# Kernel tuning notes

Hardware: AMD Instinct MI355X
Metric: run time of the kernel (lower is better)

The kernel has to match this reference:

```python
import jax, jax.numpy as jnp
import numpy as np

F_DIM = 128
H_DIM = 128
T_DIM = H_DIM // 4          # 32
D = H_DIM + T_DIM           # 160, block hidden dim
N_NODES = 100000
N_EDGES = 800000
N_LAYERS = 2
LN_EPS = 1e-5


def _layernorm(x, g, b):
    m = jnp.mean(x, axis=-1, keepdims=True)
    v = jnp.mean(jnp.square(x - m), axis=-1, keepdims=True)
    return (x - m) * jax.lax.rsqrt(v + LN_EPS) * g + b


def setup_inputs() -> dict:
    key = jax.random.key(0)
    ks = jax.random.split(key, 24)
    p = lambda k, shape: jax.random.normal(k, shape, dtype=jnp.float32) * 0.05
    inp = {
        "node_features": jax.random.normal(ks[0], (N_NODES, F_DIM), dtype=jnp.float32),
        "edge_index": jax.random.randint(ks[1], (2, N_EDGES), 0, N_NODES, dtype=jnp.int32),
        "edge_weights": jax.random.uniform(ks[2], (N_EDGES,), dtype=jnp.float32),
        "time_steps": jax.random.uniform(ks[3], (N_NODES, 1), dtype=jnp.float32),
        # node encoder: Linear(F,H) + LN(H)
        "w_enc": p(ks[4], (H_DIM, F_DIM)), "b_enc": jnp.zeros((H_DIM,)),
        "g_enc": jnp.ones((H_DIM,)), "be_enc": jnp.zeros((H_DIM,)),
        # time encoder: Linear(1,T) + LN(T)
        "w_time": p(ks[5], (T_DIM, 1)), "b_time": jnp.zeros((T_DIM,)),
        "g_time": jnp.ones((T_DIM,)), "be_time": jnp.zeros((T_DIM,)),
        # per-layer block params (stacked over layers)
        "wm": p(ks[6], (N_LAYERS, D, 2 * D)), "bm": jnp.zeros((N_LAYERS, D)),
        "gm": jnp.ones((N_LAYERS, D)), "bem": jnp.zeros((N_LAYERS, D)),
        "wu": p(ks[7], (N_LAYERS, D, 2 * D)), "bu": jnp.zeros((N_LAYERS, D)),
        "gu": jnp.ones((N_LAYERS, D)), "beu": jnp.zeros((N_LAYERS, D)),
        "wg": p(ks[8], (N_LAYERS, 1, D)), "bg": jnp.zeros((N_LAYERS, 1)),
        # output projection Linear(D, F)
        "w_out": p(ks[9], (F_DIM, D)), "b_out": jnp.zeros((F_DIM,)),
    }
    return inp


def _block(h, src, dst, w, wm, bm, gm, bem, wu, bu, gu, beu, wg, bg):
    n = h.shape[0]
    # gather endpoints -> per-edge message MLP -> weight -> scatter-add mean
    ecat = jnp.concatenate([h[src], h[dst]], axis=-1)              # [E, 2D]
    em = jax.nn.relu(_layernorm(ecat @ wm.T + bm, gm, bem)) * w[:, None]
    msum = jax.ops.segment_sum(em, dst, num_segments=n)            # [N, D]
    cnt = jax.ops.segment_sum(jnp.ones_like(w), dst, num_segments=n)[:, None]
    valid = (cnt > 0).astype(h.dtype)
    messages = msum / (cnt + 1e-8) * valid
    tw = jax.nn.sigmoid(h @ wg.T + bg)                             # [N, 1]
    h_new = jax.nn.relu(_layernorm(jnp.concatenate([h, messages], axis=-1) @ wu.T + bu, gu, beu))
    return tw * h_new + (1 - tw) * h


def reference(node_features, edge_index, edge_weights, time_steps,
              w_enc, b_enc, g_enc, be_enc, w_time, b_time, g_time, be_time,
              wm, bm, gm, bem, wu, bu, gu, beu, wg, bg, w_out, b_out):
    src, dst = edge_index[0], edge_index[1]
    h = jax.nn.relu(_layernorm(node_features @ w_enc.T + b_enc, g_enc, be_enc))
    t = jax.nn.relu(_layernorm(time_steps @ w_time.T + b_time, g_time, be_time))
    h_t = jnp.concatenate([h, t], axis=-1)                          # [N, D]
    for l in range(N_LAYERS):
        h_t = _block(h_t, src, dst, edge_weights,
                     wm[l], bm[l], gm[l], bem[l],
                     wu[l], bu[l], gu[l], beu[l], wg[l], bg[l])
    out = h_t @ w_out.T + b_out
    # F.normalize(dim=-1), eps=1e-12
    norm = jnp.linalg.norm(out, axis=-1, keepdims=True)
    return out / jnp.maximum(norm, 1e-12)
```

## Files before the change

### kernel.cpp

```cpp
#include <hip/hip_runtime.h>

#define NN 100000
#define NE 800000

typedef _Float16 half8 __attribute__((ext_vector_type(8)));
typedef _Float16 half4 __attribute__((ext_vector_type(4)));
typedef float floatx4 __attribute__((ext_vector_type(4)));

__global__ __launch_bounds__(256) void k_zero(float4* __restrict__ p, int n4) {
  int i = blockIdx.x * 256 + threadIdx.x;
  if (i < n4) p[i] = make_float4(0.f, 0.f, 0.f, 0.f);
}

__global__ __launch_bounds__(256) void k_pack(
    const float* __restrict__ w_enc, const float* __restrict__ w_out,
    const float* __restrict__ wu, const float* __restrict__ wm,
    _Float16* __restrict__ WeP, _Float16* __restrict__ WoP,
    _Float16* __restrict__ WuP, _Float16* __restrict__ WpP) {
  int gid = blockIdx.x * 256 + threadIdx.x;
  int fid = gid >> 6, lane = gid & 63;
  int mrow = lane & 15, quad = lane >> 4;
  const float* src; _Float16* dst; int stride, NI, f, g;
  if (fid < 32) {
    f = fid; g = f; src = w_enc; dst = WeP; stride = 128; NI = 8;
  } else if (fid < 72) {
    f = fid - 32; g = f; src = w_out; dst = WoP; stride = 160; NI = 8;
  } else if (fid < 272) {
    f = fid - 72; g = f % 100; src = wu + (f / 100) * 51200; dst = WuP; stride = 320; NI = 10;
  } else {
    f = fid - 272; g = f % 50;
    int l = f / 100, h = (f % 100) / 50;
    src = wm + l * 51200 + h * 160; dst = WpP; stride = 320; NI = 10;
  }
  int kk = g / NI, i = g - kk * NI;
  const float* sp = src + (size_t)(i * 16 + mrow) * stride + kk * 32 + quad * 8;
  float4 f0 = *(const float4*)sp;
  float4 f1 = *(const float4*)(sp + 4);
  half8 v = {(_Float16)f0.x, (_Float16)f0.y, (_Float16)f0.z, (_Float16)f0.w,
             (_Float16)f1.x, (_Float16)f1.y, (_Float16)f1.z, (_Float16)f1.w};
  *(half8*)&dst[(size_t)(f * 64 + lane) * 8] = v;
}

__global__ __launch_bounds__(256) void k_count_i(const int* __restrict__ ei,
                                                 int* __restrict__ cnti) {
  int e = blockIdx.x * 256 + threadIdx.x;
  atomicAdd(&cnti[ei[NE + e]], 1);
}

__global__ __launch_bounds__(256) void k_scan1(const int* __restrict__ cnti,
                                               int* __restrict__ off,
                                               int* __restrict__ bsum) {
  __shared__ int sh[256];
  const int t = threadIdx.x;
  const int i = blockIdx.x * 256 + t;
  int v = (i < NN) ? cnti[i] : 0;
  sh[t] = v;
  __syncthreads();
  for (int d = 1; d < 256; d <<= 1) {
    int add = (t >= d) ? sh[t - d] : 0;
    __syncthreads();
    sh[t] += add;
    __syncthreads();
  }
  if (i < NN) off[i] = sh[t] - v;
  if (t == 255) bsum[blockIdx.x] = sh[255];
}

__global__ __launch_bounds__(512) void k_scan2(const int* __restrict__ bsum,
                                               int* __restrict__ bsum2) {
  __shared__ int sh[512];
  const int t = threadIdx.x;
  int v = (t < 391) ? bsum[t] : 0;
  sh[t] = v;
  __syncthreads();
  for (int d = 1; d < 512; d <<= 1) {
    int add = (t >= d) ? sh[t - d] : 0;
    __syncthreads();
    sh[t] += add;
    __syncthreads();
  }
  if (t < 391) bsum2[t] = sh[t] - v;
}

__global__ __launch_bounds__(256) void k_scan3(int* __restrict__ off,
                                               const int* __restrict__ bsum2,
                                               int* __restrict__ cursor) {
  const int i = blockIdx.x * 256 + threadIdx.x;
  if (i < NN) {
    int o = off[i] + bsum2[blockIdx.x];
    off[i] = o;
    cursor[i] = o;
  }
  if (i == 0) off[NN] = NE;
}

__global__ __launch_bounds__(256) void k_scatter(const int* __restrict__ ei,
                                                 const float* __restrict__ ew,
                                                 int* __restrict__ cursor,
                                                 int2* __restrict__ selist) {
  int e = blockIdx.x * 256 + threadIdx.x;
  int dst = ei[NE + e];
  int pos = atomicAdd(&cursor[dst], 1);
  selist[pos] = make_int2(ei[e], __float_as_int(ew[e]));
}

__device__ __forceinline__ void phase2_proj(
    const _Float16* __restrict__ WpP, const float* __restrict__ bm,
    _Float16* __restrict__ P, const _Float16* tile,
    int lane, int w, int mrow, int quad, int n0) {
#pragma unroll 1
  for (int half_ = 0; half_ < 2; ++half_) {
    const _Float16* Wf = WpP + half_ * 25600 + lane * 8;
    floatx4 acc2[10];
#pragma unroll
    for (int i = 0; i < 10; ++i) acc2[i] = (floatx4)0.f;
#pragma unroll
    for (int kk = 0; kk < 5; ++kk) {
      half8 a = *(const half8*)&tile[(w * 16 + mrow) * 168 + kk * 32 + quad * 8];
#pragma unroll
      for (int i = 0; i < 10; ++i) {
        half8 b = *(const half8*)&Wf[(kk * 10 + i) * 512];
        acc2[i] = __builtin_amdgcn_mfma_f32_16x16x32_f16(a, b, acc2[i], 0, 0, 0);
      }
    }
#pragma unroll
    for (int r = 0; r < 4; ++r) {
      const int row = quad * 4 + r;
      const int node = n0 + w * 16 + row;
      if (node < NN) {
        _Float16* prow = &P[(size_t)node * 320 + half_ * 160];
#pragma unroll
        for (int i = 0; i < 10; ++i) {
          int jj = i * 16 + mrow;
          prow[jj] = (_Float16)(acc2[i][r] + (half_ ? bm[jj] : 0.f));
        }
      }
    }
  }
}

__device__ __forceinline__ void write_h16(_Float16* __restrict__ h16,
                                          const _Float16* tile, int n0, int t) {
#pragma unroll
  for (int u = 0; u < 5; ++u) {
    int c = t + u * 512;
    int row = c / 20, col = (c - row * 20) * 8;
    int node = n0 + row;
    if (node < NN)
      *(half8*)&h16[(size_t)node * 160 + col] = *(const half8*)&tile[row * 168 + col];
  }
}

__global__ __launch_bounds__(512, 4) void k_encode_proj(
    const float* __restrict__ x, const float* __restrict__ tsp,
    const _Float16* __restrict__ WeP,
    const float* __restrict__ b_enc, const float* __restrict__ g_enc,
    const float* __restrict__ be_enc,
    const float* __restrict__ w_time, const float* __restrict__ b_time,
    const float* __restrict__ g_time, const float* __restrict__ be_time,
    const _Float16* __restrict__ WpP, const float* __restrict__ bm,
    _Float16* __restrict__ h16, _Float16* __restrict__ P) {
  __shared__ _Float16 tile[128 * 168];
  const int t = threadIdx.x;
  const int lane = t & 63, w = t >> 6;
  const int mrow = lane & 15, quad = lane >> 4;
  const int n0 = blockIdx.x * 128;
  int arow = n0 + w * 16 + mrow; if (arow > NN - 1) arow = NN - 1;
  const float* xrow = x + (size_t)arow * 128;
  half8 areg[4];
#pragma unroll
  for (int kt = 0; kt < 4; ++kt) {
    const int k0 = kt * 32 + quad * 8;
    float4 f0 = *(const float4*)&xrow[k0];
    float4 f1 = *(const float4*)&xrow[k0 + 4];
    half8 a = {(_Float16)f0.x, (_Float16)f0.y, (_Float16)f0.z, (_Float16)f0.w,
               (_Float16)f1.x, (_Float16)f1.y, (_Float16)f1.z, (_Float16)f1.w};
    areg[kt] = a;
  }
  float mw = 0.f, mb = 0.f;
  for (int d = 0; d < 32; ++d) { mw += w_time[d]; mb += b_time[d]; }
  mw *= (1.f / 32.f); mb *= (1.f / 32.f);
  float A = 0.f, B = 0.f, C = 0.f;
  for (int d = 0; d < 32; ++d) {
    float a = w_time[d] - mw, c = b_time[d] - mb;
    A = fmaf(a, a, A); B = fmaf(a, c, B); C = fmaf(c, c, C);
  }
  A *= (1.f / 32.f); B *= (1.f / 32.f); C *= (1.f / 32.f);
  floatx4 acc[8];
#pragma unroll
  for (int i = 0; i < 8; ++i) acc[i] = (floatx4)0.f;
  const _Float16* Wf = WeP + lane * 8;
#pragma unroll
  for (int kk = 0; kk < 4; ++kk) {
    half8 a = areg[kk];
#pragma unroll
    for (int i = 0; i < 8; ++i) {
      half8 b = *(const half8*)&Wf[(kk * 8 + i) * 512];
      acc[i] = __builtin_amdgcn_mfma_f32_16x16x32_f16(a, b, acc[i], 0, 0, 0);
    }
  }
#pragma unroll
  for (int r = 0; r < 4; ++r) {
    const int row = quad * 4 + r;
    float v[8], s = 0.f, ss = 0.f;
#pragma unroll
    for (int i = 0; i < 8; ++i) {
      v[i] = acc[i][r] + b_enc[i * 16 + mrow];
      s += v[i]; ss = fmaf(v[i], v[i], ss);
    }
#pragma unroll
    for (int off = 1; off < 16; off <<= 1) { s += __shfl_xor(s, off); ss += __shfl_xor(ss, off); }
    const float m = s * (1.f / 128.f);
    const float rs = rsqrtf(ss * (1.f / 128.f) - m * m + 1e-5f);
#pragma unroll
    for (int i = 0; i < 8; ++i) {
      int j = i * 16 + mrow;
      tile[(w * 16 + row) * 168 + j] =
          (_Float16)fmaxf(fmaf((v[i] - m) * rs, g_enc[j], be_enc[j]), 0.f);
    }
  }
#pragma unroll
  for (int rr = 0; rr < 8; ++rr) {
    int q = lane + rr * 64;
    int nn = q >> 5, d = q & 31;
    int node = n0 + w * 16 + nn;
    int nodec = (node > NN - 1) ? NN - 1 : node;
    float tsv = tsp[nodec];
    float mt = fmaf(mw, tsv, mb);
    float rst = rsqrtf(fmaf(fmaf(A, tsv, 2.f * B), tsv, C) + 1e-5f);
    float vv = fmaf(w_time[d], tsv, b_time[d]);
    float y = fmaxf(fmaf((vv - mt) * rst, g_time[d], be_time[d]), 0.f);
    tile[(w * 16 + nn) * 168 + 128 + d] = (_Float16)y;
  }
  __syncthreads();
  write_h16(h16, tile, n0, t);
  phase2_proj(WpP, bm, P, tile, lane, w, mrow, quad, n0);
}

__global__ __launch_bounds__(256) void k_edge3(
    const _Float16* __restrict__ P, const int* __restrict__ off,
    const int2* __restrict__ selist,
    const float* __restrict__ gm, const float* __restrict__ bem,
    _Float16* __restrict__ msum16) {
  const int t = threadIdx.x;
  const int jg = t & 31, g = t >> 5;
  const int n = blockIdx.x * 8 + g;
  float gmv[5], bev[5], pdv[5];
#pragma unroll
  for (int i = 0; i < 4; ++i) { gmv[i] = gm[4 * jg + i]; bev[i] = bem[4 * jg + i]; }
  gmv[4] = gm[128 + jg]; bev[4] = bem[128 + jg];
  const _Float16* pd = P + (size_t)n * 320 + 160;
  half4 pdh = *(const half4*)&pd[4 * jg];
  pdv[0] = (float)pdh.x; pdv[1] = (float)pdh.y; pdv[2] = (float)pdh.z; pdv[3] = (float)pdh.w;
  pdv[4] = (float)pd[128 + jg];
  float acc[5] = {0.f, 0.f, 0.f, 0.f, 0.f};
  const int e0 = off[n], e1 = off[n + 1];
  int k = e0;
  for (; k + 1 < e1; k += 2) {
    int2 seA = selist[k], seB = selist[k + 1];
    const _Float16* psA = P + (size_t)seA.x * 320;
    const _Float16* psB = P + (size_t)seB.x * 320;
    const float weA = __int_as_float(seA.y), weB = __int_as_float(seB.y);
    half4 a4 = *(const half4*)&psA[4 * jg];
    half4 b4 = *(const half4*)&psB[4 * jg];
    float a5 = (float)psA[128 + jg], b5 = (float)psB[128 + jg];
    float vA[5], vB[5];
    vA[0] = (float)a4.x + pdv[0]; vA[1] = (float)a4.y + pdv[1];
    vA[2] = (float)a4.z + pdv[2]; vA[3] = (float)a4.w + pdv[3]; vA[4] = a5 + pdv[4];
    vB[0] = (float)b4.x + pdv[0]; vB[1] = (float)b4.y + pdv[1];
    vB[2] = (float)b4.z + pdv[2]; vB[3] = (float)b4.w + pdv[3]; vB[4] = b5 + pdv[4];
    float sA = 0.f, ssA = 0.f, sB = 0.f, ssB = 0.f;
#pragma unroll
    for (int i = 0; i < 5; ++i) {
      sA += vA[i]; ssA = fmaf(vA[i], vA[i], ssA);
      sB += vB[i]; ssB = fmaf(vB[i], vB[i], ssB);
    }
#pragma unroll
    for (int o = 1; o < 32; o <<= 1) {
      sA += __shfl_xor(sA, o); ssA += __shfl_xor(ssA, o);
      sB += __shfl_xor(sB, o); ssB += __shfl_xor(ssB, o);
    }
    const float mA = sA * (1.f / 160.f), mB = sB * (1.f / 160.f);
    const float rsA = rsqrtf(ssA * (1.f / 160.f) - mA * mA + 1e-5f);
    const float rsB = rsqrtf(ssB * (1.f / 160.f) - mB * mB + 1e-5f);
#pragma unroll
    for (int i = 0; i < 5; ++i) {
      acc[i] = fmaf(fmaxf(fmaf((vA[i] - mA) * rsA, gmv[i], bev[i]), 0.f), weA, acc[i]);
      acc[i] = fmaf(fmaxf(fmaf((vB[i] - mB) * rsB, gmv[i], bev[i]), 0.f), weB, acc[i]);
    }
  }
  if (k < e1) {
    int2 se = selist[k];
    const _Float16* ps = P + (size_t)se.x * 320;
    const float we = __int_as_float(se.y);
    half4 s4 = *(const half4*)&ps[4 * jg];
    float v[5], s = 0.f, ss = 0.f;
    v[0] = (float)s4.x + pdv[0]; v[1] = (float)s4.y + pdv[1];
    v[2] = (float)s4.z + pdv[2]; v[3] = (float)s4.w + pdv[3];
    v[4] = (float)ps[128 + jg] + pdv[4];
#pragma unroll
    for (int i = 0; i < 5; ++i) { s += v[i]; ss = fmaf(v[i], v[i], ss); }
#pragma unroll
    for (int o = 1; o < 32; o <<= 1) { s += __shfl_xor(s, o); ss += __shfl_xor(ss, o); }
    const float m = s * (1.f / 160.f);
    const float rs = rsqrtf(ss * (1.f / 160.f) - m * m + 1e-5f);
#pragma unroll
    for (int i = 0; i < 5; ++i)
      acc[i] = fmaf(fmaxf(fmaf((v[i] - m) * rs, gmv[i], bev[i]), 0.f), we, acc[i]);
  }
  const float c = (float)(e1 - e0);
  const float ic = (c > 0.f) ? 1.f / (c + 1e-8f) : 0.f;
  _Float16* orow = msum16 + (size_t)n * 160;
  half4 o4 = {(_Float16)(acc[0] * ic), (_Float16)(acc[1] * ic),
              (_Float16)(acc[2] * ic), (_Float16)(acc[3] * ic)};
  *(half4*)&orow[4 * jg] = o4;
  orow[128 + jg] = (_Float16)(acc[4] * ic);
}

__global__ __launch_bounds__(512, 4) void k_update_proj(
    _Float16* __restrict__ h16, const _Float16* __restrict__ msum16,
    const _Float16* __restrict__ WuP, const float* __restrict__ bu,
    const float* __restrict__ gu, const float* __restrict__ beu,
    const float* __restrict__ wg, const float* __restrict__ bg,
    const _Float16* __restrict__ WpP, const float* __restrict__ bm,
    _Float16* __restrict__ P) {
  __shared__ _Float16 tile[128 * 168];
  const int t = threadIdx.x;
  const int lane = t & 63, w = t >> 6;
  const int mrow = lane & 15, quad = lane >> 4;
  const int n0 = blockIdx.x * 128;
  int arow = n0 + w * 16 + mrow; if (arow > NN - 1) arow = NN - 1;
  const _Float16* hrowp = h16 + (size_t)arow * 160;
  const _Float16* mrowp = msum16 + (size_t)arow * 160;
  half8 areg[10];
#pragma unroll
  for (int kt = 0; kt < 5; ++kt) areg[kt] = *(const half8*)&hrowp[kt * 32 + quad * 8];
#pragma unroll
  for (int kt = 5; kt < 10; ++kt) areg[kt] = *(const half8*)&mrowp[kt * 32 + quad * 8 - 160];
  float gp = 0.f;
#pragma unroll
  for (int kt = 0; kt < 5; ++kt) {
    const int k0 = kt * 32 + quad * 8;
    float4 g0 = *(const float4*)&wg[k0];
    float4 g1 = *(const float4*)&wg[k0 + 4];
    gp = fmaf((float)areg[kt][0], g0.x, gp); gp = fmaf((float)areg[kt][1], g0.y, gp);
    gp = fmaf((float)areg[kt][2], g0.z, gp); gp = fmaf((float)areg[kt][3], g0.w, gp);
    gp = fmaf((float)areg[kt][4], g1.x, gp); gp = fmaf((float)areg[kt][5], g1.y, gp);
    gp = fmaf((float)areg[kt][6], g1.z, gp); gp = fmaf((float)areg[kt][7], g1.w, gp);
  }
  gp += __shfl_xor(gp, 16); gp += __shfl_xor(gp, 32);
  const float twv = 1.f / (1.f + expf(-(gp + bg[0])));
  floatx4 acc[10];
#pragma unroll
  for (int i = 0; i < 10; ++i) acc[i] = (floatx4)0.f;
  const _Float16* Wf = WuP + lane * 8;
#pragma unroll
  for (int kk = 0; kk < 10; ++kk) {
    half8 a = areg[kk];
#pragma unroll
    for (int i = 0; i < 10; ++i) {
      half8 b = *(const half8*)&Wf[(kk * 10 + i) * 512];
      acc[i] = __builtin_amdgcn_mfma_f32_16x16x32_f16(a, b, acc[i], 0, 0, 0);
    }
  }
#pragma unroll
  for (int r = 0; r < 4; ++r) {
    const int row = quad * 4 + r;
    const int node = n0 + w * 16 + row;
    const int nodec = (node > NN - 1) ? NN - 1 : node;
    float v[10], s = 0.f, ss = 0.f;
#pragma unroll
    for (int i = 0; i < 10; ++i) {
      v[i] = acc[i][r] + bu[i * 16 + mrow];
      s += v[i]; ss = fmaf(v[i], v[i], ss);
    }
#pragma unroll
    for (int off = 1; off < 16; off <<= 1) { s += __shfl_xor(s, off); ss += __shfl_xor(ss, off); }
    const float m = s * (1.f / 160.f);
    const float rs = rsqrtf(ss * (1.f / 160.f) - m * m + 1e-5f);
    const float g = __shfl(twv, row);
    const _Float16* hr = h16 + (size_t)nodec * 160;
#pragma unroll
    for (int i = 0; i < 10; ++i) {
      int j = i * 16 + mrow;
      float hnew = fmaxf(fmaf((v[i] - m) * rs, gu[j], beu[j]), 0.f);
      float hold = (float)hr[j];
      tile[(w * 16 + row) * 168 + j] = (_Float16)fmaf(g, hnew - hold, hold);
    }
  }
  __syncthreads();
  write_h16(h16, tile, n0, t);
  phase2_proj(WpP, bm, P, tile, lane, w, mrow, quad, n0);
}

__global__ __launch_bounds__(512, 4) void k_update_out(
    const _Float16* __restrict__ h16, const _Float16* __restrict__ msum16,
    const _Float16* __restrict__ WuP, const float* __restrict__ bu,
    const float* __restrict__ gu, const float* __restrict__ beu,
    const float* __restrict__ wg, const float* __restrict__ bg,
    const _Float16* __restrict__ WoP, const float* __restrict__ b_out,
    float* __restrict__ out) {
  __shared__ _Float16 tile[128 * 168];
  const int t = threadIdx.x;
  const int lane = t & 63, w = t >> 6;
  const int mrow = lane & 15, quad = lane >> 4;
  const int n0 = blockIdx.x * 128;
  int arow = n0 + w * 16 + mrow; if (arow > NN - 1) arow = NN - 1;
  const _Float16* hrowp = h16 + (size_t)arow * 160;
  const _Float16* mrowp = msum16 + (size_t)arow * 160;
  half8 areg[10];
#pragma unroll
  for (int kt = 0; kt < 5; ++kt) areg[kt] = *(const half8*)&hrowp[kt * 32 + quad * 8];
#pragma unroll
  for (int kt = 5; kt < 10; ++kt) areg[kt] = *(const half8*)&mrowp[kt * 32 + quad * 8 - 160];
  float gp = 0.f;
#pragma unroll
  for (int kt = 0; kt < 5; ++kt) {
    const int k0 = kt * 32 + quad * 8;
    float4 g0 = *(const float4*)&wg[k0];
    float4 g1 = *(const float4*)&wg[k0 + 4];
    gp = fmaf((float)areg[kt][0], g0.x, gp); gp = fmaf((float)areg[kt][1], g0.y, gp);
    gp = fmaf((float)areg[kt][2], g0.z, gp); gp = fmaf((float)areg[kt][3], g0.w, gp);
    gp = fmaf((float)areg[kt][4], g1.x, gp); gp = fmaf((float)areg[kt][5], g1.y, gp);
    gp = fmaf((float)areg[kt][6], g1.z, gp); gp = fmaf((float)areg[kt][7], g1.w, gp);
  }
  gp += __shfl_xor(gp, 16); gp += __shfl_xor(gp, 32);
  const float twv = 1.f / (1.f + expf(-(gp + bg[0])));
  floatx4 acc[10];
#pragma unroll
  for (int i = 0; i < 10; ++i) acc[i] = (floatx4)0.f;
  const _Float16* Wf = WuP + lane * 8;
#pragma unroll
  for (int kk = 0; kk < 10; ++kk) {
    half8 a = areg[kk];
#pragma unroll
    for (int i = 0; i < 10; ++i) {
      half8 b = *(const half8*)&Wf[(kk * 10 + i) * 512];
      acc[i] = __builtin_amdgcn_mfma_f32_16x16x32_f16(a, b, acc[i], 0, 0, 0);
    }
  }
#pragma unroll
  for (int r = 0; r < 4; ++r) {
    const int row = quad * 4 + r;
    const int node = n0 + w * 16 + row;
    const int nodec = (node > NN - 1) ? NN - 1 : node;
    float v[10], s = 0.f, ss = 0.f;
#pragma unroll
    for (int i = 0; i < 10; ++i) {
      v[i] = acc[i][r] + bu[i * 16 + mrow];
      s += v[i]; ss = fmaf(v[i], v[i], ss);
    }
#pragma unroll
    for (int off = 1; off < 16; off <<= 1) { s += __shfl_xor(s, off); ss += __shfl_xor(ss, off); }
    const float m = s * (1.f / 160.f);
    const float rs = rsqrtf(ss * (1.f / 160.f) - m * m + 1e-5f);
    const float g = __shfl(twv, row);
    const _Float16* hr = h16 + (size_t)nodec * 160;
#pragma unroll
    for (int i = 0; i < 10; ++i) {
      int j = i * 16 + mrow;
      float hnew = fmaxf(fmaf((v[i] - m) * rs, gu[j], beu[j]), 0.f);
      float hold = (float)hr[j];
      tile[(w * 16 + row) * 168 + j] = (_Float16)fmaf(g, hnew - hold, hold);
    }
  }
  __syncthreads();
  floatx4 acc2[8];
#pragma unroll
  for (int i = 0; i < 8; ++i) acc2[i] = (floatx4)0.f;
  const _Float16* Wf2 = WoP + lane * 8;
#pragma unroll
  for (int kk = 0; kk < 5; ++kk) {
    half8 a = *(const half8*)&tile[(w * 16 + mrow) * 168 + kk * 32 + quad * 8];
#pragma unroll
    for (int i = 0; i < 8; ++i) {
      half8 b = *(const half8*)&Wf2[(kk * 8 + i) * 512];
      acc2[i] = __builtin_amdgcn_mfma_f32_16x16x32_f16(a, b, acc2[i], 0, 0, 0);
    }
  }
#pragma unroll
  for (int r = 0; r < 4; ++r) {
    const int row = quad * 4 + r;
    const int node = n0 + w * 16 + row;
    float v[8], ss = 0.f;
#pragma unroll
    for (int i = 0; i < 8; ++i) {
      v[i] = acc2[i][r] + b_out[i * 16 + mrow];
      ss = fmaf(v[i], v[i], ss);
    }
#pragma unroll
    for (int off = 1; off < 16; off <<= 1) ss += __shfl_xor(ss, off);
    const float inv = 1.f / fmaxf(sqrtf(ss), 1e-12f);
    if (node < NN) {
#pragma unroll
      for (int i = 0; i < 8; ++i)
        out[(size_t)node * 128 + i * 16 + mrow] = v[i] * inv;
    }
  }
}

extern "C" void kernel_launch(void* const* d_in, const int* in_sizes, int n_in,
                              void* d_out, int out_size, void* d_ws, size_t ws_size,
                              hipStream_t stream) {
  (void)in_sizes; (void)n_in; (void)out_size; (void)ws_size;
  const float* x       = (const float*)d_in[0];
  const int*   ei      = (const int*)  d_in[1];
  const float* ew      = (const float*)d_in[2];
  const float* tsp     = (const float*)d_in[3];
  const float* w_enc   = (const float*)d_in[4];
  const float* b_enc   = (const float*)d_in[5];
  const float* g_enc   = (const float*)d_in[6];
  const float* be_enc  = (const float*)d_in[7];
  const float* w_time  = (const float*)d_in[8];
  const float* b_time  = (const float*)d_in[9];
  const float* g_time  = (const float*)d_in[10];
  const float* be_time = (const float*)d_in[11];
  const float* wm      = (const float*)d_in[12];
  const float* bm      = (const float*)d_in[13];
  const float* gm      = (const float*)d_in[14];
  const float* bem     = (const float*)d_in[15];
  const float* wu      = (const float*)d_in[16];
  const float* bu      = (const float*)d_in[17];
  const float* gu      = (const float*)d_in[18];
  const float* beu     = (const float*)d_in[19];
  const float* wg      = (const float*)d_in[20];
  const float* bg      = (const float*)d_in[21];
  const float* w_out   = (const float*)d_in[22];
  const float* b_out   = (const float*)d_in[23];
  float* out = (float*)d_out;

  char* ws = (char*)d_ws;
  _Float16* h16    = (_Float16*)ws;
  _Float16* msum16 = (_Float16*)(ws + 32000000);
  _Float16* P      = (_Float16*)(ws + 64000000);
  _Float16* WuP16  = (_Float16*)(ws + 128000000);
  _Float16* WoP16  = (_Float16*)(ws + 128204800);
  char* ob = (char*)d_out;
  _Float16* WpP16 = (_Float16*)ob;
  _Float16* WeP16 = (_Float16*)(ob + 204800);
  int* off    = (int*)(ob + 237568);
  int* cnti   = (int*)(ob + 637584);
  int* cursor = (int*)(ob + 1037584);
  int* bsum   = (int*)(ob + 1437584);
  int* bsum2  = (int*)(ob + 1439152);
  int2* selist = (int2*)(ob + 1440720);

  k_zero<<<dim3(98), dim3(256), 0, stream>>>((float4*)cnti, 25000);
  k_pack<<<dim3(118), dim3(256), 0, stream>>>(w_enc, w_out, wu, wm,
                                              WeP16, WoP16, WuP16, WpP16);
  k_count_i<<<dim3(3125), dim3(256), 0, stream>>>(ei, cnti);
  k_scan1<<<dim3(391), dim3(256), 0, stream>>>(cnti, off, bsum);
  k_scan2<<<dim3(1), dim3(512), 0, stream>>>(bsum, bsum2);
  k_scan3<<<dim3(391), dim3(256), 0, stream>>>(off, bsum2, cursor);
  k_scatter<<<dim3(3125), dim3(256), 0, stream>>>(ei, ew, cursor, selist);

  k_encode_proj<<<dim3(782), dim3(512), 0, stream>>>(
      x, tsp, WeP16, b_enc, g_enc, be_enc, w_time, b_time, g_time, be_time,
      WpP16, bm, h16, P);
  k_edge3<<<dim3(12500), dim3(256), 0, stream>>>(P, off, selist, gm, bem, msum16);
  k_update_proj<<<dim3(782), dim3(512), 0, stream>>>(
      h16, msum16, WuP16, bu, gu, beu, wg, bg,
      WpP16 + 51200, bm + 160, P);
  k_edge3<<<dim3(12500), dim3(256), 0, stream>>>(P, off, selist, gm + 160, bem + 160, msum16);
  k_update_out<<<dim3(782), dim3(512), 0, stream>>>(
      h16, msum16, WuP16 + 51200, bu + 160, gu + 160, beu + 160, wg + 160, bg + 1,
      WoP16, b_out, out);
}
```

Before: 592.9 us.

## Process two 16-row M tiles per wave and software-pipeline weight fragment loads

```diff
diff --git a/kernel.cpp b/kernel.cpp
--- a/kernel.cpp
+++ b/kernel.cpp
@@ -6,6 +6,9 @@
 typedef _Float16 half8 __attribute__((ext_vector_type(8)));
 typedef _Float16 half4 __attribute__((ext_vector_type(4)));
 typedef float floatx4 __attribute__((ext_vector_type(4)));
+
+#define LDB(Wf, f) (*(const half8*)&(Wf)[(f) * 512])
+#define BSEL(g) (((g) & 3) == 0 ? b0 : ((g) & 3) == 1 ? b1 : ((g) & 3) == 2 ? b2 : b3)
 
 __global__ __launch_bounds__(256) void k_zero(float4* __restrict__ p, int n4) {
   int i = blockIdx.x * 256 + threadIdx.x;
@@ -104,54 +107,186 @@
   selist[pos] = make_int2(ei[e], __float_as_int(ew[e]));
 }
 
-__device__ __forceinline__ void phase2_proj(
+__device__ __forceinline__ half8 cvt8(const float* p) {
+  float4 f0 = *(const float4*)p;
+  float4 f1 = *(const float4*)(p + 4);
+  half8 a = {(_Float16)f0.x, (_Float16)f0.y, (_Float16)f0.z, (_Float16)f0.w,
+             (_Float16)f1.x, (_Float16)f1.y, (_Float16)f1.z, (_Float16)f1.w};
+  return a;
+}
+
+__device__ __forceinline__ void write_h16(_Float16* __restrict__ h16,
+                                          const _Float16* tile, int n0, int t) {
+#pragma unroll
+  for (int u = 0; u < 10; ++u) {
+    int c = t + u * 256;
+    int row = c / 20, col = (c - row * 20) * 8;
+    int node = n0 + row;
+    if (node < NN)
+      *(half8*)&h16[(size_t)node * 160 + col] = *(const half8*)&tile[row * 168 + col];
+  }
+}
+
+__device__ __forceinline__ void phase2_proj_2m(
     const _Float16* __restrict__ WpP, const float* __restrict__ bm,
     _Float16* __restrict__ P, const _Float16* tile,
     int lane, int w, int mrow, int quad, int n0) {
 #pragma unroll 1
   for (int half_ = 0; half_ < 2; ++half_) {
     const _Float16* Wf = WpP + half_ * 25600 + lane * 8;
-    floatx4 acc2[10];
-#pragma unroll
-    for (int i = 0; i < 10; ++i) acc2[i] = (floatx4)0.f;
+    floatx4 acc0[10], acc1[10];
+#pragma unroll
+    for (int i = 0; i < 10; ++i) { acc0[i] = (floatx4)0.f; acc1[i] = (floatx4)0.f; }
+    half8 b0[5], b1[5], b2[5], b3[5];
+#pragma unroll
+    for (int i = 0; i < 5; ++i) b0[i] = LDB(Wf, i);
+#pragma unroll
+    for (int i = 0; i < 5; ++i) b1[i] = LDB(Wf, 5 + i);
+#pragma unroll
+    for (int i = 0; i < 5; ++i) b2[i] = LDB(Wf, 10 + i);
 #pragma unroll
     for (int kk = 0; kk < 5; ++kk) {
-      half8 a = *(const half8*)&tile[(w * 16 + mrow) * 168 + kk * 32 + quad * 8];
+      half8 a0 = *(const half8*)&tile[(w * 32 + mrow) * 168 + kk * 32 + quad * 8];
+      half8 a1 = *(const half8*)&tile[(w * 32 + 16 + mrow) * 168 + kk * 32 + quad * 8];
+#pragma unroll
+      for (int hh = 0; hh < 2; ++hh) {
+        const int g = kk * 2 + hh;
+        if (g + 3 < 10) {
+          half8* bn = BSEL(g + 3);
+#pragma unroll
+          for (int i = 0; i < 5; ++i) bn[i] = LDB(Wf, (g + 3) * 5 + i);
+        }
+        half8* bc = BSEL(g);
+#pragma unroll
+        for (int i = 0; i < 5; ++i) {
+          acc0[hh * 5 + i] = __builtin_amdgcn_mfma_f32_16x16x32_f16(a0, bc[i], acc0[hh * 5 + i], 0, 0, 0);
+          acc1[hh * 5 + i] = __builtin_amdgcn_mfma_f32_16x16x32_f16(a1, bc[i], acc1[hh * 5 + i], 0, 0, 0);
+        }
+      }
+    }
+#pragma unroll
+    for (int s = 0; s < 2; ++s) {
+#pragma unroll
+      for (int r = 0; r < 4; ++r) {
+        const int row = w * 32 + s * 16 + quad * 4 + r;
+        const int node = n0 + row;
+        if (node < NN) {
+          _Float16* prow = &P[(size_t)node * 320 + half_ * 160];
+#pragma unroll
+          for (int i = 0; i < 10; ++i) {
+            int jj = i * 16 + mrow;
+            float vv = (s ? acc1[i][r] : acc0[i][r]) + (half_ ? bm[jj] : 0.f);
+            prow[jj] = (_Float16)vv;
+          }
+        }
+      }
+    }
+  }
+}
+
+__device__ __forceinline__ void update_phase1(
+    const _Float16* __restrict__ h16, const _Float16* __restrict__ msum16,
+    const _Float16* __restrict__ WuP, const float* __restrict__ bu,
+    const float* __restrict__ gu, const float* __restrict__ beu,
+    const float* __restrict__ wg, const float* __restrict__ bg,
+    _Float16* tile, int lane, int w, int mrow, int quad, int n0) {
+  int arow0 = n0 + w * 32 + mrow; if (arow0 > NN - 1) arow0 = NN - 1;
+  int arow1 = arow0 + 16; if (arow1 > NN - 1) arow1 = NN - 1;
+  const _Float16* h0 = h16 + (size_t)arow0 * 160;
+  const _Float16* h1 = h16 + (size_t)arow1 * 160;
+  const _Float16* ms0 = msum16 + (size_t)arow0 * 160;
+  const _Float16* ms1 = msum16 + (size_t)arow1 * 160;
+  const _Float16* Wf = WuP + lane * 8;
+  half8 b0[5], b1[5], b2[5], b3[5];
+#pragma unroll
+  for (int i = 0; i < 5; ++i) b0[i] = LDB(Wf, i);
+#pragma unroll
+  for (int i = 0; i < 5; ++i) b1[i] = LDB(Wf, 5 + i);
+#pragma unroll
+  for (int i = 0; i < 5; ++i) b2[i] = LDB(Wf, 10 + i);
+  float gp0 = 0.f, gp1 = 0.f;
+#pragma unroll
+  for (int kt = 0; kt < 5; ++kt) {
+    half8 ha = *(const half8*)&h0[kt * 32 + quad * 8];
+    half8 hb = *(const half8*)&h1[kt * 32 + quad * 8];
+    float4 g0 = *(const float4*)&wg[kt * 32 + quad * 8];
+    float4 g1 = *(const float4*)&wg[kt * 32 + quad * 8 + 4];
+    gp0 = fmaf((float)ha[0], g0.x, gp0); gp0 = fmaf((float)ha[1], g0.y, gp0);
+    gp0 = fmaf((float)ha[2], g0.z, gp0); gp0 = fmaf((float)ha[3], g0.w, gp0);
+    gp0 = fmaf((float)ha[4], g1.x, gp0); gp0 = fmaf((float)ha[5], g1.y, gp0);
+    gp0 = fmaf((float)ha[6], g1.z, gp0); gp0 = fmaf((float)ha[7], g1.w, gp0);
+    gp1 = fmaf((float)hb[0], g0.x, gp1); gp1 = fmaf((float)hb[1], g0.y, gp1);
+    gp1 = fmaf((float)hb[2], g0.z, gp1); gp1 = fmaf((float)hb[3], g0.w, gp1);
+    gp1 = fmaf((float)hb[4], g1.x, gp1); gp1 = fmaf((float)hb[5], g1.y, gp1);
+    gp1 = fmaf((float)hb[6], g1.z, gp1); gp1 = fmaf((float)hb[7], g1.w, gp1);
+  }
+  gp0 += __shfl_xor(gp0, 16); gp0 += __shfl_xor(gp0, 32);
+  gp1 += __shfl_xor(gp1, 16); gp1 += __shfl_xor(gp1, 32);
+  const float twv0 = 1.f / (1.f + expf(-(gp0 + bg[0])));
+  const float twv1 = 1.f / (1.f + expf(-(gp1 + bg[0])));
+  floatx4 acc0[10], acc1[10];
+#pragma unroll
+  for (int i = 0; i < 10; ++i) { acc0[i] = (floatx4)0.f; acc1[i] = (floatx4)0.f; }
+  half8 a0c = *(const half8*)&h0[quad * 8];
+  half8 a1c = *(const half8*)&h1[quad * 8];
+  half8 a0n = a0c, a1n = a1c;
+#pragma unroll
+  for (int kk = 0; kk < 10; ++kk) {
+    if (kk < 9) {
+      const _Float16* p0 = (kk + 1 < 5) ? h0 + (kk + 1) * 32 : ms0 + (kk - 4) * 32;
+      const _Float16* p1 = (kk + 1 < 5) ? h1 + (kk + 1) * 32 : ms1 + (kk - 4) * 32;
+      a0n = *(const half8*)&p0[quad * 8];
+      a1n = *(const half8*)&p1[quad * 8];
+    }
+#pragma unroll
+    for (int hh = 0; hh < 2; ++hh) {
+      const int g = kk * 2 + hh;
+      if (g + 3 < 20) {
+        half8* bn = BSEL(g + 3);
+#pragma unroll
+        for (int i = 0; i < 5; ++i) bn[i] = LDB(Wf, (g + 3) * 5 + i);
+      }
+      half8* bc = BSEL(g);
+#pragma unroll
+      for (int i = 0; i < 5; ++i) {
+        acc0[hh * 5 + i] = __builtin_amdgcn_mfma_f32_16x16x32_f16(a0c, bc[i], acc0[hh * 5 + i], 0, 0, 0);
+        acc1[hh * 5 + i] = __builtin_amdgcn_mfma_f32_16x16x32_f16(a1c, bc[i], acc1[hh * 5 + i], 0, 0, 0);
+      }
+    }
+    a0c = a0n; a1c = a1n;
+  }
+#pragma unroll
+  for (int s = 0; s < 2; ++s) {
+    const float tw = s ? twv1 : twv0;
+#pragma unroll
+    for (int r = 0; r < 4; ++r) {
+      const int row = w * 32 + s * 16 + quad * 4 + r;
+      const int node = n0 + row;
+      const int nodec = (node > NN - 1) ? NN - 1 : node;
+      float v[10], sm = 0.f, ssm = 0.f;
 #pragma unroll
       for (int i = 0; i < 10; ++i) {
-        half8 b = *(const half8*)&Wf[(kk * 10 + i) * 512];
-        acc2[i] = __builtin_amdgcn_mfma_f32_16x16x32_f16(a, b, acc2[i], 0, 0, 0);
-      }
-    }
-#pragma unroll
-    for (int r = 0; r < 4; ++r) {
-      const int row = quad * 4 + r;
-      const int node = n0 + w * 16 + row;
-      if (node < NN) {
-        _Float16* prow = &P[(size_t)node * 320 + half_ * 160];
-#pragma unroll
-        for (int i = 0; i < 10; ++i) {
-          int jj = i * 16 + mrow;
-          prow[jj] = (_Float16)(acc2[i][r] + (half_ ? bm[jj] : 0.f));
-        }
-      }
-    }
-  }
-}
-
-__device__ __forceinline__ void write_h16(_Float16* __restrict__ h16,
-                                          const _Float16* tile, int n0, int t) {
-#pragma unroll
-  for (int u = 0; u < 5; ++u) {
-    int c = t + u * 512;
-    int row = c / 20, col = (c - row * 20) * 8;
-    int node = n0 + row;
-    if (node < NN)
-      *(half8*)&h16[(size_t)node * 160 + col] = *(const half8*)&tile[row * 168 + col];
-  }
-}
-
-__global__ __launch_bounds__(512, 4) void k_encode_proj(
+        v[i] = (s ? acc1[i][r] : acc0[i][r]) + bu[i * 16 + mrow];
+        sm += v[i]; ssm = fmaf(v[i], v[i], ssm);
+      }
+#pragma unroll
+      for (int off = 1; off < 16; off <<= 1) { sm += __shfl_xor(sm, off); ssm += __shfl_xor(ssm, off); }
+      const float m = sm * (1.f / 160.f);
+      const float rs = rsqrtf(ssm * (1.f / 160.f) - m * m + 1e-5f);
+      const float g = __shfl(tw, quad * 4 + r);
+      const _Float16* hr = h16 + (size_t)nodec * 160;
+#pragma unroll
+      for (int i = 0; i < 10; ++i) {
+        int j = i * 16 + mrow;
+        float hnew = fmaxf(fmaf((v[i] - m) * rs, gu[j], beu[j]), 0.f);
+        float hold = (float)hr[j];
+        tile[row * 168 + j] = (_Float16)fmaf(g, hnew - hold, hold);
+      }
+    }
+  }
+}
+
+__global__ __launch_bounds__(256, 2) void k_encode_proj(
     const float* __restrict__ x, const float* __restrict__ tsp,
     const _Float16* __restrict__ WeP,
     const float* __restrict__ b_enc, const float* __restrict__ g_enc,
@@ -165,18 +300,14 @@
   const int lane = t & 63, w = t >> 6;
   const int mrow = lane & 15, quad = lane >> 4;
   const int n0 = blockIdx.x * 128;
-  int arow = n0 + w * 16 + mrow; if (arow > NN - 1) arow = NN - 1;
-  const float* xrow = x + (size_t)arow * 128;
-  half8 areg[4];
-#pragma unroll
-  for (int kt = 0; kt < 4; ++kt) {
-    const int k0 = kt * 32 + quad * 8;
-    float4 f0 = *(const float4*)&xrow[k0];
-    float4 f1 = *(const float4*)&xrow[k0 + 4];
-    half8 a = {(_Float16)f0.x, (_Float16)f0.y, (_Float16)f0.z, (_Float16)f0.w,
-               (_Float16)f1.x, (_Float16)f1.y, (_Float16)f1.z, (_Float16)f1.w};
-    areg[kt] = a;
-  }
+  int arow0 = n0 + w * 32 + mrow; if (arow0 > NN - 1) arow0 = NN - 1;
+  int arow1 = arow0 + 16; if (arow1 > NN - 1) arow1 = NN - 1;
+  const float* xr0 = x + (size_t)arow0 * 128;
+  const float* xr1 = x + (size_t)arow1 * 128;
+  const _Float16* Wf = WeP + lane * 8;
+  half8 b0[8], b1[8];
+#pragma unroll
+  for (int i = 0; i < 8; ++i) b0[i] = LDB(Wf, i);
   float mw = 0.f, mb = 0.f;
   for (int d = 0; d < 32; ++d) { mw += w_time[d]; mb += b_time[d]; }
   mw *= (1.f / 32.f); mb *= (1.f / 32.f);
@@ -186,55 +317,68 @@
     A = fmaf(a, a, A); B = fmaf(a, c, B); C = fmaf(c, c, C);
   }
   A *= (1.f / 32.f); B *= (1.f / 32.f); C *= (1.f / 32.f);
-  floatx4 acc[8];
-#pragma unroll
-  for (int i = 0; i < 8; ++i) acc[i] = (floatx4)0.f;
-  const _Float16* Wf = WeP + lane * 8;
+  floatx4 acc0[8], acc1[8];
+#pragma unroll
+  for (int i = 0; i < 8; ++i) { acc0[i] = (floatx4)0.f; acc1[i] = (floatx4)0.f; }
+  half8 a0c = cvt8(&xr0[quad * 8]);
+  half8 a1c = cvt8(&xr1[quad * 8]);
+  half8 a0n = a0c, a1n = a1c;
 #pragma unroll
   for (int kk = 0; kk < 4; ++kk) {
-    half8 a = areg[kk];
+    if (kk < 3) {
+      half8* bn = (kk & 1) ? b0 : b1;
+#pragma unroll
+      for (int i = 0; i < 8; ++i) bn[i] = LDB(Wf, (kk + 1) * 8 + i);
+      a0n = cvt8(&xr0[(kk + 1) * 32 + quad * 8]);
+      a1n = cvt8(&xr1[(kk + 1) * 32 + quad * 8]);
+    }
+    half8* bc = (kk & 1) ? b1 : b0;
 #pragma unroll
     for (int i = 0; i < 8; ++i) {
-      half8 b = *(const half8*)&Wf[(kk * 8 + i) * 512];
-      acc[i] = __builtin_amdgcn_mfma_f32_16x16x32_f16(a, b, acc[i], 0, 0, 0);
-    }
-  }
-#pragma unroll
-  for (int r = 0; r < 4; ++r) {
-    const int row = quad * 4 + r;
-    float v[8], s = 0.f, ss = 0.f;
-#pragma unroll
-    for (int i = 0; i < 8; ++i) {
-      v[i] = acc[i][r] + b_enc[i * 16 + mrow];
-      s += v[i]; ss = fmaf(v[i], v[i], ss);
-    }
-#pragma unroll
-    for (int off = 1; off < 16; off <<= 1) { s += __shfl_xor(s, off); ss += __shfl_xor(ss, off); }
-    const float m = s * (1.f / 128.f);
-    const float rs = rsqrtf(ss * (1.f / 128.f) - m * m + 1e-5f);
-#pragma unroll
-    for (int i = 0; i < 8; ++i) {
-      int j = i * 16 + mrow;
-      tile[(w * 16 + row) * 168 + j] =
-          (_Float16)fmaxf(fmaf((v[i] - m) * rs, g_enc[j], be_enc[j]), 0.f);
-    }
-  }
-#pragma unroll
-  for (int rr = 0; rr < 8; ++rr) {
+      acc0[i] = __builtin_amdgcn_mfma_f32_16x16x32_f16(a0c, bc[i], acc0[i], 0, 0, 0);
+      acc1[i] = __builtin_amdgcn_mfma_f32_16x16x32_f16(a1c, bc[i], acc1[i], 0, 0, 0);
+    }
+    a0c = a0n; a1c = a1n;
+  }
+#pragma unroll
+  for (int s = 0; s < 2; ++s) {
+#pragma unroll
+    for (int r = 0; r < 4; ++r) {
+      const int row = w * 32 + s * 16 + quad * 4 + r;
+      float v[8], sm = 0.f, ssm = 0.f;
+#pragma unroll
+      for (int i = 0; i < 8; ++i) {
+        v[i] = (s ? acc1[i][r] : acc0[i][r]) + b_enc[i * 16 + mrow];
+        sm += v[i]; ssm = fmaf(v[i], v[i], ssm);
+      }
+#pragma unroll
+      for (int off = 1; off < 16; off <<= 1) { sm += __shfl_xor(sm, off); ssm += __shfl_xor(ssm, off); }
+      const float m = sm * (1.f / 128.f);
+      const float rs = rsqrtf(ssm * (1.f / 128.f) - m * m + 1e-5f);
+#pragma unroll
+      for (int i = 0; i < 8; ++i) {
+        int j = i * 16 + mrow;
+        tile[row * 168 + j] =
+            (_Float16)fmaxf(fmaf((v[i] - m) * rs, g_enc[j], be_enc[j]), 0.f);
+      }
+    }
+  }
+#pragma unroll
+  for (int rr = 0; rr < 16; ++rr) {
     int q = lane + rr * 64;
     int nn = q >> 5, d = q & 31;
-    int node = n0 + w * 16 + nn;
+    int node = n0 + w * 32 + nn;
     int nodec = (node > NN - 1) ? NN - 1 : node;
     float tsv = tsp[nodec];
     float mt = fmaf(mw, tsv, mb);
     float rst = rsqrtf(fmaf(fmaf(A, tsv, 2.f * B), tsv, C) + 1e-5f);
     float vv = fmaf(w_time[d], tsv, b_time[d]);
     float y = fmaxf(fmaf((vv - mt) * rst, g_time[d], be_time[d]), 0.f);
-    tile[(w * 16 + nn) * 168 + 128 + d] = (_Float16)y;
+    tile[(w * 32 + nn) * 168 + 128 + d] = (_Float16)y;
   }
   __syncthreads();
   write_h16(h16, tile, n0, t);
-  phase2_proj(WpP, bm, P, tile, lane, w, mrow, quad, n0);
+  phase2_proj_2m(WpP, bm, P, tile, lane, w, mrow, quad, n0);
 }
 
 __global__ __launch_bounds__(256) void k_edge3(
@@ -317,7 +461,7 @@
   orow[128 + jg] = (_Float16)(acc[4] * ic);
 }
 
-__global__ __launch_bounds__(512, 4) void k_update_proj(
+__global__ __launch_bounds__(256, 2) void k_update_proj(
     _Float16* __restrict__ h16, const _Float16* __restrict__ msum16,
     const _Float16* __restrict__ WuP, const float* __restrict__ bu,
     const float* __restrict__ gu, const float* __restrict__ beu,
@@ -329,71 +473,13 @@
   const int lane = t & 63, w = t >> 6;
   const int mrow = lane & 15, quad = lane >> 4;
   const int n0 = blockIdx.x * 128;
-  int arow = n0 + w * 16 + mrow; if (arow > NN - 1) arow = NN - 1;
-  const _Float16* hrowp = h16 + (size_t)arow * 160;
-  const _Float16* mrowp = msum16 + (size_t)arow * 160;
-  half8 areg[10];
-#pragma unroll
-  for (int kt = 0; kt < 5; ++kt) areg[kt] = *(const half8*)&hrowp[kt * 32 + quad * 8];
-#pragma unroll
-  for (int kt = 5; kt < 10; ++kt) areg[kt] = *(const half8*)&mrowp[kt * 32 + quad * 8 - 160];
-  float gp = 0.f;
-#pragma unroll
-  for (int kt = 0; kt < 5; ++kt) {
-    const int k0 = kt * 32 + quad * 8;
-    float4 g0 = *(const float4*)&wg[k0];
-    float4 g1 = *(const float4*)&wg[k0 + 4];
-    gp = fmaf((float)areg[kt][0], g0.x, gp); gp = fmaf((float)areg[kt][1], g0.y, gp);
-    gp = fmaf((float)areg[kt][2], g0.z, gp); gp = fmaf((float)areg[kt][3], g0.w, gp);
-    gp = fmaf((float)areg[kt][4], g1.x, gp); gp = fmaf((float)areg[kt][5], g1.y, gp);
-    gp = fmaf((float)areg[kt][6], g1.z, gp); gp = fmaf((float)areg[kt][7], g1.w, gp);
-  }
-  gp += __shfl_xor(gp, 16); gp += __shfl_xor(gp, 32);
-  const float twv = 1.f / (1.f + expf(-(gp + bg[0])));
-  floatx4 acc[10];
-#pragma unroll
-  for (int i = 0; i < 10; ++i) acc[i] = (floatx4)0.f;
-  const _Float16* Wf = WuP + lane * 8;
-#pragma unroll
-  for (int kk = 0; kk < 10; ++kk) {
-    half8 a = areg[kk];
-#pragma unroll
-    for (int i = 0; i < 10; ++i) {
-      half8 b = *(const half8*)&Wf[(kk * 10 + i) * 512];
-      acc[i] = __builtin_amdgcn_mfma_f32_16x16x32_f16(a, b, acc[i], 0, 0, 0);
-    }
-  }
-#pragma unroll
-  for (int r = 0; r < 4; ++r) {
-    const int row = quad * 4 + r;
-    const int node = n0 + w * 16 + row;
-    const int nodec = (node > NN - 1) ? NN - 1 : node;
-    float v[10], s = 0.f, ss = 0.f;
-#pragma unroll
-    for (int i = 0; i < 10; ++i) {
-      v[i] = acc[i][r] + bu[i * 16 + mrow];
-      s += v[i]; ss = fmaf(v[i], v[i], ss);
-    }
-#pragma unroll
-    for (int off = 1; off < 16; off <<= 1) { s += __shfl_xor(s, off); ss += __shfl_xor(ss, off); }
-    const float m = s * (1.f / 160.f);
-    const float rs = rsqrtf(ss * (1.f / 160.f) - m * m + 1e-5f);
-    const float g = __shfl(twv, row);
-    const _Float16* hr = h16 + (size_t)nodec * 160;
-#pragma unroll
-    for (int i = 0; i < 10; ++i) {
-      int j = i * 16 + mrow;
-      float hnew = fmaxf(fmaf((v[i] - m) * rs, gu[j], beu[j]), 0.f);
-      float hold = (float)hr[j];
-      tile[(w * 16 + row) * 168 + j] = (_Float16)fmaf(g, hnew - hold, hold);
-    }
-  }
+  update_phase1(h16, msum16, WuP, bu, gu, beu, wg, bg, tile, lane, w, mrow, quad, n0);
   __syncthreads();
   write_h16(h16, tile, n0, t);
-  phase2_proj(WpP, bm, P, tile, lane, w, mrow, quad, n0);
-}
-
-__global__ __launch_bounds__(512, 4) void k_update_out(
+  phase2_proj_2m(WpP, bm, P, tile, lane, w, mrow, quad, n0);
+}
+
+__global__ __launch_bounds__(256, 2) void k_update_out(
     const _Float16* __restrict__ h16, const _Float16* __restrict__ msum16,
     const _Float16* __restrict__ WuP, const float* __restrict__ bu,
     const float* __restrict__ gu, const float* __restrict__ beu,
@@ -405,96 +491,50 @@
   const int lane = t & 63, w = t >> 6;
   const int mrow = lane & 15, quad = lane >> 4;
   const int n0 = blockIdx.x * 128;
-  int arow = n0 + w * 16 + mrow; if (arow > NN - 1) arow = NN - 1;
-  const _Float16* hrowp = h16 + (size_t)arow * 160;
-  const _Float16* mrowp = msum16 + (size_t)arow * 160;
-  half8 areg[10];
-#pragma unroll
-  for (int kt = 0; kt < 5; ++kt) areg[kt] = *(const half8*)&hrowp[kt * 32 + quad * 8];
-#pragma unroll
-  for (int kt = 5; kt < 10; ++kt) areg[kt] = *(const half8*)&mrowp[kt * 32 + quad * 8 - 160];
-  float gp = 0.f;
-#pragma unroll
-  for (int kt = 0; kt < 5; ++kt) {
-    const int k0 = kt * 32 + quad * 8;
-    float4 g0 = *(const float4*)&wg[k0];
-    float4 g1 = *(const float4*)&wg[k0 + 4];
-    gp = fmaf((float)areg[kt][0], g0.x, gp); gp = fmaf((float)areg[kt][1], g0.y, gp);
-    gp = fmaf((float)areg[kt][2], g0.z, gp); gp = fmaf((float)areg[kt][3], g0.w, gp);
-    gp = fmaf((float)areg[kt][4], g1.x, gp); gp = fmaf((float)areg[kt][5], g1.y, gp);
-    gp = fmaf((float)areg[kt][6], g1.z, gp); gp = fmaf((float)areg[kt][7], g1.w, gp);
-  }
-  gp += __shfl_xor(gp, 16); gp += __shfl_xor(gp, 32);
-  const float twv = 1.f / (1.f + expf(-(gp + bg[0])));
-  floatx4 acc[10];
-#pragma unroll
-  for (int i = 0; i < 10; ++i) acc[i] = (floatx4)0.f;
-  const _Float16* Wf = WuP + lane * 8;
-#pragma unroll
-  for (int kk = 0; kk < 10; ++kk) {
-    half8 a = areg[kk];
-#pragma unroll
-    for (int i = 0; i < 10; ++i) {
-      half8 b = *(const half8*)&Wf[(kk * 10 + i) * 512];
-      acc[i] = __builtin_amdgcn_mfma_f32_16x16x32_f16(a, b, acc[i], 0, 0, 0);
-    }
-  }
-#pragma unroll
-  for (int r = 0; r < 4; ++r) {
-    const int row = quad * 4 + r;
-    const int node = n0 + w * 16 + row;
-    const int nodec = (node > NN - 1) ? NN - 1 : node;
-    float v[10], s = 0.f, ss = 0.f;
-#pragma unroll
-    for (int i = 0; i < 10; ++i) {
-      v[i] = acc[i][r] + bu[i * 16 + mrow];
-      s += v[i]; ss = fmaf(v[i], v[i], ss);
-    }
-#pragma unroll
-    for (int off = 1; off < 16; off <<= 1) { s += __shfl_xor(s, off); ss += __shfl_xor(ss, off); }
-    const float m = s * (1.f / 160.f);
-    const float rs = rsqrtf(ss * (1.f / 160.f) - m * m + 1e-5f);
-    const float g = __shfl(twv, row);
-    const _Float16* hr = h16 + (size_t)nodec * 160;
-#pragma unroll
-    for (int i = 0; i < 10; ++i) {
-      int j = i * 16 + mrow;
-      float hnew = fmaxf(fmaf((v[i] - m) * rs, gu[j], beu[j]), 0.f);
-      float hold = (float)hr[j];
-      tile[(w * 16 + row) * 168 + j] = (_Float16)fmaf(g, hnew - hold, hold);
-    }
-  }
-  __syncthreads();
-  floatx4 acc2[8];
-#pragma unroll
-  for (int i = 0; i < 8; ++i) acc2[i] = (floatx4)0.f;
-  const _Float16* Wf2 = WoP + lane * 8;
+  update_phase1(h16, msum16, WuP, bu, gu, beu, wg, bg, tile, lane, w, mrow, quad, n0);
+  const _Float16* Wf = WoP + lane * 8;
+  half8 b0[8], b1[8];
+#pragma unroll
+  for (int i = 0; i < 8; ++i) b0[i] = LDB(Wf, i);
+  floatx4 acc0[8], acc1[8];
+#pragma unroll
+  for (int i = 0; i < 8; ++i) { acc0[i] = (floatx4)0.f; acc1[i] = (floatx4)0.f; }
 #pragma unroll
   for (int kk = 0; kk < 5; ++kk) {
-    half8 a = *(const half8*)&tile[(w * 16 + mrow) * 168 + kk * 32 + quad * 8];
+    if (kk < 4) {
+      half8* bn = (kk & 1) ? b0 : b1;
+#pragma unroll
+      for (int i = 0; i < 8; ++i) bn[i] = LDB(Wf, (kk + 1) * 8 + i);
+    }
+    half8 a0 = *(const half8*)&tile[(w * 32 + mrow) * 168 + kk * 32 + quad * 8];
+    half8 a1 = *(const half8*)&tile[(w * 32 + 16 + mrow) * 168 + kk * 32 + quad * 8];
+    half8* bc = (kk & 1) ? b1 : b0;
 #pragma unroll
     for (int i = 0; i < 8; ++i) {
-      half8 b = *(const half8*)&Wf2[(kk * 8 + i) * 512];
-      acc2[i] = __builtin_amdgcn_mfma_f32_16x16x32_f16(a, b, acc2[i], 0, 0, 0);
-    }
-  }
-#pragma unroll
-  for (int r = 0; r < 4; ++r) {
-    const int row = quad * 4 + r;
-    const int node = n0 + w * 16 + row;
-    float v[8], ss = 0.f;
-#pragma unroll
-    for (int i = 0; i < 8; ++i) {
-      v[i] = acc2[i][r] + b_out[i * 16 + mrow];
-      ss = fmaf(v[i], v[i], ss);
-    }
-#pragma unroll
-    for (int off = 1; off < 16; off <<= 1) ss += __shfl_xor(ss, off);
-    const float inv = 1.f / fmaxf(sqrtf(ss), 1e-12f);
-    if (node < NN) {
-#pragma unroll
-      for (int i = 0; i < 8; ++i)
-        out[(size_t)node * 128 + i * 16 + mrow] = v[i] * inv;
+      acc0[i] = __builtin_amdgcn_mfma_f32_16x16x32_f16(a0, bc[i], acc0[i], 0, 0, 0);
+      acc1[i] = __builtin_amdgcn_mfma_f32_16x16x32_f16(a1, bc[i], acc1[i], 0, 0, 0);
+    }
+  }
+#pragma unroll
+  for (int s = 0; s < 2; ++s) {
+#pragma unroll
+    for (int r = 0; r < 4; ++r) {
+      const int row = w * 32 + s * 16 + quad * 4 + r;
+      const int node = n0 + row;
+      float v[8], ssm = 0.f;
+#pragma unroll
+      for (int i = 0; i < 8; ++i) {
+        v[i] = (s ? acc1[i][r] : acc0[i][r]) + b_out[i * 16 + mrow];
+        ssm = fmaf(v[i], v[i], ssm);
+      }
+#pragma unroll
+      for (int off = 1; off < 16; off <<= 1) ssm += __shfl_xor(ssm, off);
+      const float inv = 1.f / fmaxf(sqrtf(ssm), 1e-12f);
+      if (node < NN) {
+#pragma unroll
+        for (int i = 0; i < 8; ++i)
+          out[(size_t)node * 128 + i * 16 + mrow] = v[i] * inv;
+      }
     }
   }
 }
@@ -554,15 +594,15 @@
   k_scan3<<<dim3(391), dim3(256), 0, stream>>>(off, bsum2, cursor);
   k_scatter<<<dim3(3125), dim3(256), 0, stream>>>(ei, ew, cursor, selist);
 
-  k_encode_proj<<<dim3(782), dim3(512), 0, stream>>>(
+  k_encode_proj<<<dim3(782), dim3(256), 0, stream>>>(
       x, tsp, WeP16, b_enc, g_enc, be_enc, w_time, b_time, g_time, be_time,
       WpP16, bm, h16, P);
   k_edge3<<<dim3(12500), dim3(256), 0, stream>>>(P, off, selist, gm, bem, msum16);
-  k_update_proj<<<dim3(782), dim3(512), 0, stream>>>(
+  k_update_proj<<<dim3(782), dim3(256), 0, stream>>>(
       h16, msum16, WuP16, bu, gu, beu, wg, bg,
       WpP16 + 51200, bm + 160, P);
   k_edge3<<<dim3(12500), dim3(256), 0, stream>>>(P, off, selist, gm + 160, bem + 160, msum16);
-  k_update_out<<<dim3(782), dim3(512), 0, stream>>>(
+  k_update_out<<<dim3(782), dim3(256), 0, stream>>>(
       h16, msum16, WuP16 + 51200, bu + 160, gu + 160, beu + 160, wg + 160, bg + 1,
       WoP16, b_out, out);
 }
```

New measurement: 629.9 us. +6.2%, slower.
